# Performance work log

Measured on AMD Instinct MI355X. Metric: run time of the kernel, lower is better.

The kernel has to match this reference:

```python
import jax, jax.numpy as jnp
import numpy as np

N_NODES = 50000
N_EDGES = 800000
IN_SIZE = 256
OUT_SIZE = 256


def setup_inputs() -> dict:
    key = jax.random.key(0)
    k1, k2, k3, k4, k5 = jax.random.split(key, 5)
    x = jax.random.normal(k1, (N_NODES, IN_SIZE), dtype=jnp.float32)
    # nn.Linear default init: U(-1/sqrt(in), 1/sqrt(in)); randn-scaled is fine for a numeric baseline
    bound = 1.0 / np.sqrt(IN_SIZE)
    W = jax.random.uniform(k2, (IN_SIZE, OUT_SIZE), minval=-bound, maxval=bound, dtype=jnp.float32)
    b = jax.random.uniform(k3, (OUT_SIZE,), minval=-bound, maxval=bound, dtype=jnp.float32)
    edge_src = jax.random.randint(k4, (N_EDGES,), 0, N_NODES, dtype=jnp.int32)
    edge_dst = jax.random.randint(k5, (N_EDGES,), 0, N_NODES, dtype=jnp.int32)
    return {"x": x, "W": W, "b": b, "edge_src": edge_src, "edge_dst": edge_dst}


def reference(x, W, b, edge_src, edge_dst):
    # 1) dense projection (nn.Linear):  Wh = x @ W + b   -> [N, out]
    Wh = x @ W + b
    # 2) copy_u: gather source-node projected features per edge -> [E, out]
    m = Wh[edge_src]
    # 3) mean reduce per destination node (DGL fn.mean): zero for isolated nodes
    summed = jax.ops.segment_sum(m, edge_dst, num_segments=N_NODES)  # [N, out]
    deg = jax.ops.segment_sum(jnp.ones((edge_dst.shape[0],), dtype=x.dtype),
                              edge_dst, num_segments=N_NODES)       # [N]
    h = summed / jnp.maximum(deg, 1.0)[:, None]
    return h
```

## Files before the change

### kernel.cpp

```cpp
#include <hip/hip_runtime.h>

#define NN 50000
#define NE 800000
#define DIN 256
#define DOUT 256
#define NSLICE 8
#define QPAD 32
#define ECHUNK 1024
#define NECHUNK ((NE + ECHUNK - 1) / ECHUNK)
#define DRANGE (NN / NSLICE)
#define SLOTS 32
#define OVFCAP 4096
#define PREP_BLKS 12756

typedef __attribute__((ext_vector_type(8))) short short8;
typedef __attribute__((ext_vector_type(4))) float floatx4;

static __device__ __forceinline__ unsigned short f2bf(float f) {
    unsigned int u = __float_as_uint(f);
    unsigned int r = (u + 0x7fffu + ((u >> 16) & 1u)) >> 16;
    return (unsigned short)r;
}

static __device__ __forceinline__ void gload_lds16(const void* g, void* l) {
    __builtin_amdgcn_global_load_lds(
        (const __attribute__((address_space(1))) unsigned int*)g,
        (__attribute__((address_space(3))) unsigned int*)l, 16, 0, 0);
}

__global__ void zero_ints_kernel(int* __restrict__ p, int n) {
    int i = blockIdx.x * blockDim.x + threadIdx.x;
    if (i < n) p[i] = 0;
}

__global__ __launch_bounds__(256) void work_kernel(const float* __restrict__ x,
                                                   const float* __restrict__ W,
                                                   unsigned int* __restrict__ xq,
                                                   float* __restrict__ sinv,
                                                   unsigned short* __restrict__ Wt,
                                                   const int* __restrict__ edge_src,
                                                   const int* __restrict__ edge_dst,
                                                   int* __restrict__ cnt,
                                                   int* __restrict__ qctr,
                                                   unsigned short* __restrict__ slots,
                                                   int* __restrict__ ovf_n,
                                                   int* __restrict__ ovf_d,
                                                   int* __restrict__ ovf_s) {
    int bid = blockIdx.x;
    if (bid < 12500) {
        int row = bid * 4 + (threadIdx.x >> 6);
        int lane = threadIdx.x & 63;
        float4 v = *(const float4*)(x + (size_t)row * DIN + lane * 4);
        float m = fmaxf(fmaxf(fabsf(v.x), fabsf(v.y)), fmaxf(fabsf(v.z), fabsf(v.w)));
#pragma unroll
        for (int d = 1; d < 64; d <<= 1) m = fmaxf(m, __shfl_xor(m, d));
        m = fmaxf(m, 1e-20f);
        float sc = 127.0f / m;
        int q0 = (int)rintf(v.x * sc);
        int q1 = (int)rintf(v.y * sc);
        int q2 = (int)rintf(v.z * sc);
        int q3 = (int)rintf(v.w * sc);
        unsigned int pack = (q0 & 255) | ((q1 & 255) << 8) | ((q2 & 255) << 16) | ((q3 & 255) << 24);
        xq[(size_t)row * 64 + lane] = pack;
        if (lane == 0) sinv[row] = m * (1.0f / 127.0f);
        return;
    }
    if (bid < PREP_BLKS) {
        int n = bid - 12500;
        int k = threadIdx.x;
        Wt[(size_t)n * DIN + k] = f2bf(W[(size_t)k * DOUT + n]);
        return;
    }
    __shared__ int sh;
    int xcd;
    asm("s_getreg_b32 %0, hwreg(HW_REG_XCC_ID, 0, 32)" : "=s"(xcd));
    xcd &= 7;
    int tid = threadIdx.x;
    if (tid == 0) {
        int found = -1;
        for (int t = 0; t < NSLICE; t++) {
            int q = (xcd + t) & 7;
            int c = atomicAdd(&qctr[q * QPAD], 1);
            if (c < NECHUNK) { found = q * NECHUNK + c; break; }
        }
        sh = found;
    }
    __syncthreads();
    int f = sh;
    if (f < 0) return;
    int q = f / NECHUNK;
    int chunk = f % NECHUNK;
    int dlo = q * DRANGE, dhi = dlo + DRANGE;
    int e0 = chunk * ECHUNK;
#pragma unroll
    for (int k = 0; k < ECHUNK / 256; k++) {
        int e = e0 + k * 256 + tid;
        if (e < NE) {
            int d = edge_dst[e];
            if (d >= dlo && d < dhi) {
                int src = edge_src[e];
                int pos = atomicAdd(&cnt[d], 1);
                if (pos < SLOTS) {
                    slots[(d << 5) + pos] = (unsigned short)src;
                } else {
                    int oi = atomicAdd(ovf_n, 1);
                    if (oi < OVFCAP) { ovf_d[oi] = d; ovf_s[oi] = src; }
                }
            }
        }
    }
}

__global__ __launch_bounds__(256) void mean_kernel(const unsigned int* __restrict__ xq,
                                                   const float* __restrict__ sinv,
                                                   const int* __restrict__ cnt,
                                                   const unsigned short* __restrict__ slots,
                                                   const int* __restrict__ ovf_n,
                                                   const int* __restrict__ ovf_d,
                                                   const int* __restrict__ ovf_s,
                                                   unsigned short* __restrict__ xm) {
    int node = blockIdx.x * 4 + (threadIdx.x >> 6);
    int lane = threadIdx.x & 63;
    int half = lane >> 5;
    int cg = lane & 31;
    int cv = cnt[node];
    int end = (cv < SLOTS) ? cv : SLOTS;
    const unsigned short* sp = slots + (node << 5);
    const unsigned int* xcol = xq + cg * 2;
    float a[8];
#pragma unroll
    for (int j = 0; j < 8; j++) a[j] = 0.f;
    int i = half;
    for (; i + 6 < end; i += 8) {
        int s0 = sp[i], s1 = sp[i + 2], s2 = sp[i + 4], s3 = sp[i + 6];
        float c0 = sinv[s0], c1 = sinv[s1], c2 = sinv[s2], c3 = sinv[s3];
        int2 q0 = *(const int2*)(xcol + (size_t)s0 * 64);
        int2 q1 = *(const int2*)(xcol + (size_t)s1 * 64);
        int2 q2 = *(const int2*)(xcol + (size_t)s2 * 64);
        int2 q3 = *(const int2*)(xcol + (size_t)s3 * 64);
#pragma unroll
        for (int j = 0; j < 4; j++) {
            int sh = 8 * j;
            a[j]     += c0 * (float)((signed char)(q0.x >> sh))
                      + c1 * (float)((signed char)(q1.x >> sh))
                      + c2 * (float)((signed char)(q2.x >> sh))
                      + c3 * (float)((signed char)(q3.x >> sh));
            a[4 + j] += c0 * (float)((signed char)(q0.y >> sh))
                      + c1 * (float)((signed char)(q1.y >> sh))
                      + c2 * (float)((signed char)(q2.y >> sh))
                      + c3 * (float)((signed char)(q3.y >> sh));
        }
    }
    for (; i < end; i += 2) {
        int s = sp[i];
        float c = sinv[s];
        int2 qv = *(const int2*)(xcol + (size_t)s * 64);
#pragma unroll
        for (int j = 0; j < 4; j++) {
            int sh = 8 * j;
            a[j]     += c * (float)((signed char)(qv.x >> sh));
            a[4 + j] += c * (float)((signed char)(qv.y >> sh));
        }
    }
    if (cv > SLOTS && half == 0) {
        int n = *ovf_n;
        if (n > OVFCAP) n = OVFCAP;
        for (int k = 0; k < n; k++) {
            if (ovf_d[k] == node) {
                int s = ovf_s[k];
                float c = sinv[s];
                int2 qv = *(const int2*)(xcol + (size_t)s * 64);
#pragma unroll
                for (int j = 0; j < 4; j++) {
                    int sh = 8 * j;
                    a[j]     += c * (float)((signed char)(qv.x >> sh));
                    a[4 + j] += c * (float)((signed char)(qv.y >> sh));
                }
            }
        }
    }
#pragma unroll
    for (int j = 0; j < 8; j++) a[j] += __shfl_xor(a[j], 32);
    float inv = (cv > 0) ? 1.0f / (float)cv : 0.f;
    if (half == 0) {
        short8 o;
#pragma unroll
        for (int j = 0; j < 8; j++) o[j] = (short)f2bf(a[j] * inv);
        *(short8*)(xm + (size_t)node * DIN + cg * 8) = o;
    }
}

__global__ __launch_bounds__(256) void gemm_mfma_kernel(const unsigned short* __restrict__ xm,
                                                        const unsigned short* __restrict__ Wt,
                                                        const float* __restrict__ b,
                                                        const int* __restrict__ cnt,
                                                        float* __restrict__ out) {
    __shared__ unsigned short As[128 * 32];
    __shared__ unsigned short Bs[128 * 32];
    int tid = threadIdx.x;
    int bm = blockIdx.x >> 1;
    int bn = blockIdx.x & 1;
    int row0 = bm * 128, col0 = bn * 128;
    int wave = tid >> 6, lane = tid & 63;
    int wr = wave >> 1, wc = wave & 1;
    int l15 = lane & 15, kgrp = lane >> 4;

    floatx4 acc[4][4];
#pragma unroll
    for (int m = 0; m < 4; m++)
#pragma unroll
        for (int n = 0; n < 4; n++) acc[m][n] = (floatx4){0.f, 0.f, 0.f, 0.f};

    int srow = tid >> 2;
    int kchunk = (tid & 3) * 8;

    for (int kc = 0; kc < DIN; kc += 32) {
#pragma unroll
        for (int i = 0; i < 2; i++) {
            int row = i * 64 + srow;
            int ga_row = row0 + row; if (ga_row >= NN) ga_row = NN - 1;
            gload_lds16(xm + (size_t)ga_row * DIN + kc + kchunk,
                        (char*)As + i * 4096 + wave * 1024);
            gload_lds16(Wt + (size_t)(col0 + row) * DIN + kc + kchunk,
                        (char*)Bs + i * 4096 + wave * 1024);
        }
        __syncthreads();

        short8 af[4], bf[4];
#pragma unroll
        for (int m = 0; m < 4; m++)
            af[m] = *(const short8*)&As[(wr * 64 + m * 16 + l15) * 32 + kgrp * 8];
#pragma unroll
        for (int n = 0; n < 4; n++)
            bf[n] = *(const short8*)&Bs[(wc * 64 + n * 16 + l15) * 32 + kgrp * 8];
#pragma unroll
        for (int m = 0; m < 4; m++)
#pragma unroll
            for (int n = 0; n < 4; n++)
                acc[m][n] = __builtin_amdgcn_mfma_f32_16x16x32_bf16(af[m], bf[n], acc[m][n], 0, 0, 0);
        __syncthreads();
    }

    float bias[4];
#pragma unroll
    for (int n = 0; n < 4; n++) bias[n] = b[col0 + wc * 64 + n * 16 + l15];

#pragma unroll
    for (int m = 0; m < 4; m++) {
#pragma unroll
        for (int r = 0; r < 4; r++) {
            int row = row0 + wr * 64 + m * 16 + kgrp * 4 + r;
            if (row < NN) {
                int dg = cnt[row];
#pragma unroll
                for (int n = 0; n < 4; n++) {
                    int col = col0 + wc * 64 + n * 16 + l15;
                    out[(size_t)row * DOUT + col] = (dg > 0) ? acc[m][n][r] + bias[n] : 0.f;
                }
            }
        }
    }
}

extern "C" void kernel_launch(void* const* d_in, const int* in_sizes, int n_in,
                              void* d_out, int out_size, void* d_ws, size_t ws_size,
                              hipStream_t stream) {
    const float* x = (const float*)d_in[0];
    const float* W = (const float*)d_in[1];
    const float* b = (const float*)d_in[2];
    const int* esrc = (const int*)d_in[3];
    const int* edst = (const int*)d_in[4];
    float* out = (float*)d_out;

    char* ws = (char*)d_ws;
    size_t off = 0;
    unsigned int* xq = (unsigned int*)(ws + off); off += (size_t)NN * DIN;
    unsigned short* xm = (unsigned short*)(ws + off); off += (size_t)NN * DIN * 2;
    float* sinv = (float*)(ws + off); off += (size_t)NN * sizeof(float);
    unsigned short* Wt = (unsigned short*)(ws + off); off += (size_t)DIN * DOUT * 2;
    unsigned short* slots = (unsigned short*)(ws + off); off += (size_t)NN * SLOTS * 2;
    int* cnt = (int*)(ws + off); off += (size_t)NN * sizeof(int);
    int* qctrS = (int*)(ws + off); off += (size_t)NSLICE * QPAD * sizeof(int);
    int* ovf_n = (int*)(ws + off); off += 4 * sizeof(int);
    int* ovf_d = (int*)(ws + off); off += OVFCAP * sizeof(int);
    int* ovf_s = (int*)(ws + off); off += OVFCAP * sizeof(int);

    const int nzero = NN + NSLICE * QPAD + 4;
    zero_ints_kernel<<<(nzero + 255) / 256, 256, 0, stream>>>(cnt, nzero);
    work_kernel<<<PREP_BLKS + NSLICE * NECHUNK, 256, 0, stream>>>(
        x, W, xq, sinv, Wt, esrc, edst, cnt, qctrS, slots, ovf_n, ovf_d, ovf_s);
    mean_kernel<<<NN / 4, 256, 0, stream>>>(xq, sinv, cnt, slots, ovf_n, ovf_d, ovf_s, xm);
    gemm_mfma_kernel<<<391 * 2, 256, 0, stream>>>(xm, Wt, b, cnt, out);
}
```

Measured before the change: 115.7 us.

## Bucket edges by destination slice once before per-slice scatter

```diff
diff --git a/kernel.cpp b/kernel.cpp
--- a/kernel.cpp
+++ b/kernel.cpp
@@ -6,12 +6,15 @@
 #define DOUT 256
 #define NSLICE 8
 #define QPAD 32
-#define ECHUNK 1024
-#define NECHUNK ((NE + ECHUNK - 1) / ECHUNK)
 #define DRANGE (NN / NSLICE)
 #define SLOTS 32
 #define OVFCAP 4096
 #define PREP_BLKS 12756
+#define PART_BLKS 1024
+#define EPB ((NE + PART_BLKS - 1) / PART_BLKS)
+#define BCAP 131072
+#define SCHUNK 1024
+#define MAXCH (BCAP / SCHUNK)
 
 typedef __attribute__((ext_vector_type(8))) short short8;
 typedef __attribute__((ext_vector_type(4))) float floatx4;
@@ -40,16 +43,13 @@
                                                    unsigned short* __restrict__ Wt,
                                                    const int* __restrict__ edge_src,
                                                    const int* __restrict__ edge_dst,
-                                                   int* __restrict__ cnt,
-                                                   int* __restrict__ qctr,
-                                                   unsigned short* __restrict__ slots,
-                                                   int* __restrict__ ovf_n,
-                                                   int* __restrict__ ovf_d,
-                                                   int* __restrict__ ovf_s) {
+                                                   unsigned int* __restrict__ part,
+                                                   int* __restrict__ gcur) {
     int bid = blockIdx.x;
+    int tid = threadIdx.x;
     if (bid < 12500) {
-        int row = bid * 4 + (threadIdx.x >> 6);
-        int lane = threadIdx.x & 63;
+        int row = bid * 4 + (tid >> 6);
+        int lane = tid & 63;
         float4 v = *(const float4*)(x + (size_t)row * DIN + lane * 4);
         float m = fmaxf(fmaxf(fabsf(v.x), fabsf(v.y)), fmaxf(fabsf(v.z), fabsf(v.w)));
 #pragma unroll
@@ -67,10 +67,46 @@
     }
     if (bid < PREP_BLKS) {
         int n = bid - 12500;
-        int k = threadIdx.x;
-        Wt[(size_t)n * DIN + k] = f2bf(W[(size_t)k * DOUT + n]);
+        Wt[(size_t)n * DIN + tid] = f2bf(W[(size_t)tid * DOUT + n]);
         return;
     }
+    __shared__ int lcnt[8];
+    __shared__ int lbase[8];
+    int pb = bid - PREP_BLKS;
+    int ebeg = pb * EPB;
+    int eend = ebeg + EPB; if (eend > NE) eend = NE;
+    for (int base = ebeg; base < eend; base += 256) {
+        int e = base + tid;
+        int q = -1, lrank = 0;
+        unsigned int pack = 0;
+        if (tid < 8) lcnt[tid] = 0;
+        __syncthreads();
+        if (e < eend) {
+            int d = edge_dst[e];
+            int s = edge_src[e];
+            q = d / DRANGE;
+            pack = ((unsigned int)(d - q * DRANGE) << 16) | (unsigned int)s;
+            lrank = atomicAdd(&lcnt[q], 1);
+        }
+        __syncthreads();
+        if (tid < 8) lbase[tid] = atomicAdd(&gcur[tid * QPAD], lcnt[tid]);
+        __syncthreads();
+        if (q >= 0) {
+            int pos = lbase[q] + lrank;
+            if (pos < BCAP) part[(size_t)q * BCAP + pos] = pack;
+        }
+        __syncthreads();
+    }
+}
+
+__global__ __launch_bounds__(256) void scatter2_kernel(const unsigned int* __restrict__ part,
+                                                       const int* __restrict__ gcur,
+                                                       int* __restrict__ qctr,
+                                                       int* __restrict__ cnt,
+                                                       unsigned short* __restrict__ slots,
+                                                       int* __restrict__ ovf_n,
+                                                       int* __restrict__ ovf_d,
+                                                       int* __restrict__ ovf_s) {
     __shared__ int sh;
     int xcd;
     asm("s_getreg_b32 %0, hwreg(HW_REG_XCC_ID, 0, 32)" : "=s"(xcd));
@@ -80,32 +116,35 @@
         int found = -1;
         for (int t = 0; t < NSLICE; t++) {
             int q = (xcd + t) & 7;
+            int cq = gcur[q * QPAD]; if (cq > BCAP) cq = BCAP;
+            int need = (cq + SCHUNK - 1) / SCHUNK;
             int c = atomicAdd(&qctr[q * QPAD], 1);
-            if (c < NECHUNK) { found = q * NECHUNK + c; break; }
+            if (c < need) { found = q * 256 + c; break; }
         }
         sh = found;
     }
     __syncthreads();
     int f = sh;
     if (f < 0) return;
-    int q = f / NECHUNK;
-    int chunk = f % NECHUNK;
-    int dlo = q * DRANGE, dhi = dlo + DRANGE;
-    int e0 = chunk * ECHUNK;
-#pragma unroll
-    for (int k = 0; k < ECHUNK / 256; k++) {
-        int e = e0 + k * 256 + tid;
-        if (e < NE) {
-            int d = edge_dst[e];
-            if (d >= dlo && d < dhi) {
-                int src = edge_src[e];
-                int pos = atomicAdd(&cnt[d], 1);
-                if (pos < SLOTS) {
-                    slots[(d << 5) + pos] = (unsigned short)src;
-                } else {
-                    int oi = atomicAdd(ovf_n, 1);
-                    if (oi < OVFCAP) { ovf_d[oi] = d; ovf_s[oi] = src; }
-                }
+    int q = f >> 8;
+    int c = f & 255;
+    int count = gcur[q * QPAD]; if (count > BCAP) count = BCAP;
+    const unsigned int* pp = part + (size_t)q * BCAP;
+    int base = c * SCHUNK;
+    int dbase = q * DRANGE;
+#pragma unroll
+    for (int k = 0; k < SCHUNK / 256; k++) {
+        int e = base + k * 256 + tid;
+        if (e < count) {
+            unsigned int p = pp[e];
+            int d = dbase + (int)(p >> 16);
+            int src = (int)(p & 0xffffu);
+            int pos = atomicAdd(&cnt[d], 1);
+            if (pos < SLOTS) {
+                slots[(d << 5) + pos] = (unsigned short)src;
+            } else {
+                int oi = atomicAdd(ovf_n, 1);
+                if (oi < OVFCAP) { ovf_d[oi] = d; ovf_s[oi] = src; }
             }
         }
     }
@@ -279,16 +318,20 @@
     float* sinv = (float*)(ws + off); off += (size_t)NN * sizeof(float);
     unsigned short* Wt = (unsigned short*)(ws + off); off += (size_t)DIN * DOUT * 2;
     unsigned short* slots = (unsigned short*)(ws + off); off += (size_t)NN * SLOTS * 2;
+    unsigned int* part = (unsigned int*)(ws + off); off += (size_t)NSLICE * BCAP * 4;
     int* cnt = (int*)(ws + off); off += (size_t)NN * sizeof(int);
-    int* qctrS = (int*)(ws + off); off += (size_t)NSLICE * QPAD * sizeof(int);
+    int* gcur = (int*)(ws + off); off += (size_t)NSLICE * QPAD * sizeof(int);
+    int* qctr2 = (int*)(ws + off); off += (size_t)NSLICE * QPAD * sizeof(int);
     int* ovf_n = (int*)(ws + off); off += 4 * sizeof(int);
     int* ovf_d = (int*)(ws + off); off += OVFCAP * sizeof(int);
     int* ovf_s = (int*)(ws + off); off += OVFCAP * sizeof(int);
 
-    const int nzero = NN + NSLICE * QPAD + 4;
+    const int nzero = NN + 2 * NSLICE * QPAD + 4;
     zero_ints_kernel<<<(nzero + 255) / 256, 256, 0, stream>>>(cnt, nzero);
-    work_kernel<<<PREP_BLKS + NSLICE * NECHUNK, 256, 0, stream>>>(
-        x, W, xq, sinv, Wt, esrc, edst, cnt, qctrS, slots, ovf_n, ovf_d, ovf_s);
+    work_kernel<<<PREP_BLKS + PART_BLKS, 256, 0, stream>>>(
+        x, W, xq, sinv, Wt, esrc, edst, part, gcur);
+    scatter2_kernel<<<NSLICE * 128, 256, 0, stream>>>(part, gcur, qctr2, cnt, slots,
+                                                      ovf_n, ovf_d, ovf_s);
     mean_kernel<<<NN / 4, 256, 0, stream>>>(xq, sinv, cnt, slots, ovf_n, ovf_d, ovf_s, xm);
     gemm_mfma_kernel<<<391 * 2, 256, 0, stream>>>(xm, Wt, b, cnt, out);
 }
```

Result: slower. 160.8 us (+38.9%).

## Replace per-node global atomics with two-level radix partition of edges by destination

Applied to the files above, without the earlier changes.

```diff
diff --git a/kernel.cpp b/kernel.cpp
--- a/kernel.cpp
+++ b/kernel.cpp
@@ -4,14 +4,17 @@
 #define NE 800000
 #define DIN 256
 #define DOUT 256
-#define NSLICE 8
-#define QPAD 32
-#define ECHUNK 1024
-#define NECHUNK ((NE + ECHUNK - 1) / ECHUNK)
-#define DRANGE (NN / NSLICE)
-#define SLOTS 32
+#define NR 8
+#define RSZ 6250
+#define NSUB 196
+#define SUBCAP 1024
+#define BCAP 131072
+#define A1_BLKS 256
+#define A1_EPB (NE / A1_BLKS)
+#define A2_BLKS 128
+#define QP 8
 #define OVFCAP 4096
-#define PREP_BLKS 12756
+#define WORK_GRID (A1_BLKS + 12500 + 256)
 
 typedef __attribute__((ext_vector_type(8))) short short8;
 typedef __attribute__((ext_vector_type(4))) float floatx4;
@@ -40,16 +43,41 @@
                                                    unsigned short* __restrict__ Wt,
                                                    const int* __restrict__ edge_src,
                                                    const int* __restrict__ edge_dst,
-                                                   int* __restrict__ cnt,
-                                                   int* __restrict__ qctr,
-                                                   unsigned short* __restrict__ slots,
-                                                   int* __restrict__ ovf_n,
-                                                   int* __restrict__ ovf_d,
-                                                   int* __restrict__ ovf_s) {
+                                                   unsigned int* __restrict__ part,
+                                                   int* __restrict__ gcur) {
     int bid = blockIdx.x;
-    if (bid < 12500) {
-        int row = bid * 4 + (threadIdx.x >> 6);
-        int lane = threadIdx.x & 63;
+    int tid = threadIdx.x;
+    if (bid < A1_BLKS) {
+        __shared__ int lcnt[NR];
+        __shared__ int lbase[NR];
+        int ebeg = bid * A1_EPB;
+        int eend = ebeg + A1_EPB;
+        if (tid < NR) lcnt[tid] = 0;
+        __syncthreads();
+        for (int e = ebeg + tid; e < eend; e += 256) {
+            unsigned int d = (unsigned int)edge_dst[e];
+            atomicAdd(&lcnt[d / RSZ], 1);
+        }
+        __syncthreads();
+        if (tid < NR) {
+            lbase[tid] = atomicAdd(&gcur[tid * QP], lcnt[tid]);
+            lcnt[tid] = 0;
+        }
+        __syncthreads();
+        for (int e = ebeg + tid; e < eend; e += 256) {
+            unsigned int d = (unsigned int)edge_dst[e];
+            unsigned int s = (unsigned int)edge_src[e];
+            unsigned int q = d / RSZ;
+            unsigned int dl = d - q * RSZ;
+            int r = atomicAdd(&lcnt[q], 1);
+            int pos = lbase[q] + r;
+            if (pos < BCAP) part[(size_t)q * BCAP + pos] = (dl << 16) | s;
+        }
+        return;
+    }
+    if (bid < A1_BLKS + 12500) {
+        int row = (bid - A1_BLKS) * 4 + (tid >> 6);
+        int lane = tid & 63;
         float4 v = *(const float4*)(x + (size_t)row * DIN + lane * 4);
         float m = fmaxf(fmaxf(fabsf(v.x), fabsf(v.y)), fmaxf(fabsf(v.z), fabsf(v.w)));
 #pragma unroll
@@ -65,128 +93,155 @@
         if (lane == 0) sinv[row] = m * (1.0f / 127.0f);
         return;
     }
-    if (bid < PREP_BLKS) {
-        int n = bid - 12500;
-        int k = threadIdx.x;
-        Wt[(size_t)n * DIN + k] = f2bf(W[(size_t)k * DOUT + n]);
-        return;
-    }
-    __shared__ int sh;
-    int xcd;
-    asm("s_getreg_b32 %0, hwreg(HW_REG_XCC_ID, 0, 32)" : "=s"(xcd));
-    xcd &= 7;
+    {
+        int n = bid - (A1_BLKS + 12500);
+        Wt[(size_t)n * DIN + tid] = f2bf(W[(size_t)tid * DOUT + n]);
+    }
+}
+
+__global__ __launch_bounds__(256) void subpart_kernel(const unsigned int* __restrict__ part,
+                                                      const int* __restrict__ gcur,
+                                                      int* __restrict__ scur,
+                                                      unsigned int* __restrict__ sub) {
+    __shared__ int lc[NSUB];
+    __shared__ int lb[NSUB];
+    int bid = blockIdx.x;
     int tid = threadIdx.x;
-    if (tid == 0) {
-        int found = -1;
-        for (int t = 0; t < NSLICE; t++) {
-            int q = (xcd + t) & 7;
-            int c = atomicAdd(&qctr[q * QPAD], 1);
-            if (c < NECHUNK) { found = q * NECHUNK + c; break; }
-        }
-        sh = found;
-    }
-    __syncthreads();
-    int f = sh;
-    if (f < 0) return;
-    int q = f / NECHUNK;
-    int chunk = f % NECHUNK;
-    int dlo = q * DRANGE, dhi = dlo + DRANGE;
-    int e0 = chunk * ECHUNK;
-#pragma unroll
-    for (int k = 0; k < ECHUNK / 256; k++) {
-        int e = e0 + k * 256 + tid;
-        if (e < NE) {
-            int d = edge_dst[e];
-            if (d >= dlo && d < dhi) {
-                int src = edge_src[e];
-                int pos = atomicAdd(&cnt[d], 1);
-                if (pos < SLOTS) {
-                    slots[(d << 5) + pos] = (unsigned short)src;
-                } else {
-                    int oi = atomicAdd(ovf_n, 1);
-                    if (oi < OVFCAP) { ovf_d[oi] = d; ovf_s[oi] = src; }
+    int q = bid >> 4;
+    int c = bid & 15;
+    int count = gcur[q * QP]; if (count > BCAP) count = BCAP;
+    int beg = (int)(((long long)c * count) >> 4);
+    int end = (int)(((long long)(c + 1) * count) >> 4);
+    const unsigned int* pp = part + (size_t)q * BCAP;
+    if (tid < NSUB) lc[tid] = 0;
+    __syncthreads();
+    for (int i = beg + tid; i < end; i += 256) {
+        unsigned int p = pp[i];
+        atomicAdd(&lc[(p >> 16) >> 5], 1);
+    }
+    __syncthreads();
+    if (tid < NSUB) {
+        lb[tid] = atomicAdd(&scur[(q * NSUB + tid) * QP], lc[tid]);
+        lc[tid] = 0;
+    }
+    __syncthreads();
+    for (int i = beg + tid; i < end; i += 256) {
+        unsigned int p = pp[i];
+        int s = (p >> 16) >> 5;
+        int r = atomicAdd(&lc[s], 1);
+        int pos = lb[s] + r;
+        if (pos < SUBCAP) sub[((size_t)(q * NSUB + s)) * SUBCAP + pos] = p;
+    }
+}
+
+__global__ __launch_bounds__(256) void mean2_kernel(const unsigned int* __restrict__ xq,
+                                                    const float* __restrict__ sinv,
+                                                    const int* __restrict__ scur,
+                                                    const unsigned int* __restrict__ sub,
+                                                    int* __restrict__ ovf_n,
+                                                    int* __restrict__ ovf_d,
+                                                    int* __restrict__ ovf_s,
+                                                    int* __restrict__ cnt,
+                                                    unsigned short* __restrict__ xm) {
+    __shared__ unsigned short slt[32 * 64];
+    __shared__ int lcn[32];
+    int bid = blockIdx.x;
+    int tid = threadIdx.x;
+    int q = bid / NSUB;
+    int s = bid - q * NSUB;
+    int csub = scur[(q * NSUB + s) * QP]; if (csub > SUBCAP) csub = SUBCAP;
+    int n0 = q * RSZ + s * 32;
+    int nnodes = RSZ - s * 32; if (nnodes > 32) nnodes = 32;
+    const unsigned int* sp = sub + ((size_t)(q * NSUB + s)) * SUBCAP;
+
+    if (tid < 32) lcn[tid] = 0;
+    __syncthreads();
+    for (int i = tid; i < csub; i += 256) {
+        unsigned int p = sp[i];
+        int dl = (int)(p >> 16);
+        int n5 = dl & 31;
+        int pos = atomicAdd(&lcn[n5], 1);
+        if (pos < 64) slt[n5 * 64 + pos] = (unsigned short)(p & 0xffffu);
+        else {
+            int oi = atomicAdd(ovf_n, 1);
+            if (oi < OVFCAP) { ovf_d[oi] = q * RSZ + dl; ovf_s[oi] = (int)(p & 0xffffu); }
+        }
+    }
+    __syncthreads();
+
+    int wave = tid >> 6, lane = tid & 63;
+    int half = lane >> 5;
+    int cg = lane & 31;
+    const unsigned int* xcol = xq + cg * 2;
+    for (int w = 0; w < 8; w++) {
+        int n5 = wave * 8 + w;
+        if (n5 >= nnodes) break;
+        int node = n0 + n5;
+        int cv = lcn[n5];
+        int end = (cv < 64) ? cv : 64;
+        const unsigned short* sl = &slt[n5 * 64];
+        float a[8];
+#pragma unroll
+        for (int j = 0; j < 8; j++) a[j] = 0.f;
+        int i = half;
+        for (; i + 6 < end; i += 8) {
+            int s0 = sl[i], s1 = sl[i + 2], s2 = sl[i + 4], s3 = sl[i + 6];
+            float c0 = sinv[s0], c1 = sinv[s1], c2 = sinv[s2], c3 = sinv[s3];
+            int2 q0 = *(const int2*)(xcol + (size_t)s0 * 64);
+            int2 q1 = *(const int2*)(xcol + (size_t)s1 * 64);
+            int2 q2 = *(const int2*)(xcol + (size_t)s2 * 64);
+            int2 q3 = *(const int2*)(xcol + (size_t)s3 * 64);
+#pragma unroll
+            for (int j = 0; j < 4; j++) {
+                int sh = 8 * j;
+                a[j]     += c0 * (float)((signed char)(q0.x >> sh))
+                          + c1 * (float)((signed char)(q1.x >> sh))
+                          + c2 * (float)((signed char)(q2.x >> sh))
+                          + c3 * (float)((signed char)(q3.x >> sh));
+                a[4 + j] += c0 * (float)((signed char)(q0.y >> sh))
+                          + c1 * (float)((signed char)(q1.y >> sh))
+                          + c2 * (float)((signed char)(q2.y >> sh))
+                          + c3 * (float)((signed char)(q3.y >> sh));
+            }
+        }
+        for (; i < end; i += 2) {
+            int sv = sl[i];
+            float c = sinv[sv];
+            int2 qv = *(const int2*)(xcol + (size_t)sv * 64);
+#pragma unroll
+            for (int j = 0; j < 4; j++) {
+                int sh = 8 * j;
+                a[j]     += c * (float)((signed char)(qv.x >> sh));
+                a[4 + j] += c * (float)((signed char)(qv.y >> sh));
+            }
+        }
+        if (cv > 64 && half == 0) {
+            int n = *ovf_n;
+            if (n > OVFCAP) n = OVFCAP;
+            for (int k = 0; k < n; k++) {
+                if (ovf_d[k] == node) {
+                    int sv = ovf_s[k];
+                    float c = sinv[sv];
+                    int2 qv = *(const int2*)(xcol + (size_t)sv * 64);
+#pragma unroll
+                    for (int j = 0; j < 4; j++) {
+                        int sh = 8 * j;
+                        a[j]     += c * (float)((signed char)(qv.x >> sh));
+                        a[4 + j] += c * (float)((signed char)(qv.y >> sh));
+                    }
                 }
             }
         }
-    }
-}
-
-__global__ __launch_bounds__(256) void mean_kernel(const unsigned int* __restrict__ xq,
-                                                   const float* __restrict__ sinv,
-                                                   const int* __restrict__ cnt,
-                                                   const unsigned short* __restrict__ slots,
-                                                   const int* __restrict__ ovf_n,
-                                                   const int* __restrict__ ovf_d,
-                                                   const int* __restrict__ ovf_s,
-                                                   unsigned short* __restrict__ xm) {
-    int node = blockIdx.x * 4 + (threadIdx.x >> 6);
-    int lane = threadIdx.x & 63;
-    int half = lane >> 5;
-    int cg = lane & 31;
-    int cv = cnt[node];
-    int end = (cv < SLOTS) ? cv : SLOTS;
-    const unsigned short* sp = slots + (node << 5);
-    const unsigned int* xcol = xq + cg * 2;
-    float a[8];
-#pragma unroll
-    for (int j = 0; j < 8; j++) a[j] = 0.f;
-    int i = half;
-    for (; i + 6 < end; i += 8) {
-        int s0 = sp[i], s1 = sp[i + 2], s2 = sp[i + 4], s3 = sp[i + 6];
-        float c0 = sinv[s0], c1 = sinv[s1], c2 = sinv[s2], c3 = sinv[s3];
-        int2 q0 = *(const int2*)(xcol + (size_t)s0 * 64);
-        int2 q1 = *(const int2*)(xcol + (size_t)s1 * 64);
-        int2 q2 = *(const int2*)(xcol + (size_t)s2 * 64);
-        int2 q3 = *(const int2*)(xcol + (size_t)s3 * 64);
-#pragma unroll
-        for (int j = 0; j < 4; j++) {
-            int sh = 8 * j;
-            a[j]     += c0 * (float)((signed char)(q0.x >> sh))
-                      + c1 * (float)((signed char)(q1.x >> sh))
-                      + c2 * (float)((signed char)(q2.x >> sh))
-                      + c3 * (float)((signed char)(q3.x >> sh));
-            a[4 + j] += c0 * (float)((signed char)(q0.y >> sh))
-                      + c1 * (float)((signed char)(q1.y >> sh))
-                      + c2 * (float)((signed char)(q2.y >> sh))
-                      + c3 * (float)((signed char)(q3.y >> sh));
-        }
-    }
-    for (; i < end; i += 2) {
-        int s = sp[i];
-        float c = sinv[s];
-        int2 qv = *(const int2*)(xcol + (size_t)s * 64);
-#pragma unroll
-        for (int j = 0; j < 4; j++) {
-            int sh = 8 * j;
-            a[j]     += c * (float)((signed char)(qv.x >> sh));
-            a[4 + j] += c * (float)((signed char)(qv.y >> sh));
-        }
-    }
-    if (cv > SLOTS && half == 0) {
-        int n = *ovf_n;
-        if (n > OVFCAP) n = OVFCAP;
-        for (int k = 0; k < n; k++) {
-            if (ovf_d[k] == node) {
-                int s = ovf_s[k];
-                float c = sinv[s];
-                int2 qv = *(const int2*)(xcol + (size_t)s * 64);
-#pragma unroll
-                for (int j = 0; j < 4; j++) {
-                    int sh = 8 * j;
-                    a[j]     += c * (float)((signed char)(qv.x >> sh));
-                    a[4 + j] += c * (float)((signed char)(qv.y >> sh));
-                }
-            }
-        }
-    }
-#pragma unroll
-    for (int j = 0; j < 8; j++) a[j] += __shfl_xor(a[j], 32);
-    float inv = (cv > 0) ? 1.0f / (float)cv : 0.f;
-    if (half == 0) {
-        short8 o;
-#pragma unroll
-        for (int j = 0; j < 8; j++) o[j] = (short)f2bf(a[j] * inv);
-        *(short8*)(xm + (size_t)node * DIN + cg * 8) = o;
+#pragma unroll
+        for (int j = 0; j < 8; j++) a[j] += __shfl_xor(a[j], 32);
+        float inv = (cv > 0) ? 1.0f / (float)cv : 0.f;
+        if (half == 0) {
+            short8 o;
+#pragma unroll
+            for (int j = 0; j < 8; j++) o[j] = (short)f2bf(a[j] * inv);
+            *(short8*)(xm + (size_t)node * DIN + cg * 8) = o;
+        }
+        if (lane == 0) cnt[node] = cv;
     }
 }
 
@@ -278,17 +333,19 @@
     unsigned short* xm = (unsigned short*)(ws + off); off += (size_t)NN * DIN * 2;
     float* sinv = (float*)(ws + off); off += (size_t)NN * sizeof(float);
     unsigned short* Wt = (unsigned short*)(ws + off); off += (size_t)DIN * DOUT * 2;
-    unsigned short* slots = (unsigned short*)(ws + off); off += (size_t)NN * SLOTS * 2;
+    unsigned int* part = (unsigned int*)(ws + off); off += (size_t)NR * BCAP * 4;
+    unsigned int* sub = (unsigned int*)(ws + off); off += (size_t)NR * NSUB * SUBCAP * 4;
     int* cnt = (int*)(ws + off); off += (size_t)NN * sizeof(int);
-    int* qctrS = (int*)(ws + off); off += (size_t)NSLICE * QPAD * sizeof(int);
+    int* gcur = (int*)(ws + off); off += (size_t)NR * QP * sizeof(int);
+    int* scur = (int*)(ws + off); off += (size_t)NR * NSUB * QP * sizeof(int);
     int* ovf_n = (int*)(ws + off); off += 4 * sizeof(int);
     int* ovf_d = (int*)(ws + off); off += OVFCAP * sizeof(int);
     int* ovf_s = (int*)(ws + off); off += OVFCAP * sizeof(int);
 
-    const int nzero = NN + NSLICE * QPAD + 4;
+    const int nzero = NN + NR * QP + NR * NSUB * QP + 4;
     zero_ints_kernel<<<(nzero + 255) / 256, 256, 0, stream>>>(cnt, nzero);
-    work_kernel<<<PREP_BLKS + NSLICE * NECHUNK, 256, 0, stream>>>(
-        x, W, xq, sinv, Wt, esrc, edst, cnt, qctrS, slots, ovf_n, ovf_d, ovf_s);
-    mean_kernel<<<NN / 4, 256, 0, stream>>>(xq, sinv, cnt, slots, ovf_n, ovf_d, ovf_s, xm);
+    work_kernel<<<WORK_GRID, 256, 0, stream>>>(x, W, xq, sinv, Wt, esrc, edst, part, gcur);
+    subpart_kernel<<<A2_BLKS, 256, 0, stream>>>(part, gcur, scur, sub);
+    mean2_kernel<<<NR * NSUB, 256, 0, stream>>>(xq, sinv, scur, sub, ovf_n, ovf_d, ovf_s, cnt, xm);
     gemm_mfma_kernel<<<391 * 2, 256, 0, stream>>>(xm, Wt, b, cnt, out);
 }
```

Result: faster. 104.0 us (-10.2%).
